# Kernel optimization log

Measured on AMD Instinct MI355X. Metric: run time of the kernel, lower is better.

The kernel has to match this reference:

```python
import jax, jax.numpy as jnp
import numpy as np

TEMPERATURE_F = 0.5  # temperature_f from __init__


def setup_inputs() -> dict:
    key = jax.random.key(0)
    k1, k2 = jax.random.split(key)
    B, D = 4096, 512
    h_i = jax.random.normal(k1, (B, D), dtype=jnp.float32)
    h_j = jax.random.normal(k2, (B, D), dtype=jnp.float32)
    return {"h_i": h_i, "h_j": h_j}


def reference(h_i, h_j) -> jnp.ndarray:
    # NT-Xent loss (forward_private). N = 2*batch_size.
    B = h_i.shape[0]
    N = 2 * B
    h = jnp.concatenate([h_i, h_j], axis=0)          # [N, D]
    sim = (h @ h.T) / TEMPERATURE_F                   # [N, N]

    # Positive pairs: sim[i, i+B] and sim[i+B, i]
    sim_i_j = jnp.diagonal(sim, offset=B)             # [B]
    sim_j_i = jnp.diagonal(sim, offset=-B)            # [B]
    pos = jnp.concatenate([sim_i_j, sim_j_i], axis=0)  # [N]

    # Original builds logits = [pos | negatives] where negatives are the row of
    # sim with the diagonal and the positive entry removed, and labels are 0.
    # Cross-entropy per row = -pos_i + logsumexp(pos_i, negatives_i)
    #                       = -pos_i + logsumexp over row i of sim excluding the
    #                         diagonal (the positive entry equals pos_i, so the
    #                         set of logsumexp'd values is identical).
    neg_inf = jnp.finfo(sim.dtype).min
    diag = jnp.eye(N, dtype=bool)
    sim_masked = jnp.where(diag, neg_inf, sim)        # exclude self-similarity
    lse = jax.nn.logsumexp(sim_masked, axis=1)        # [N]

    loss = jnp.sum(lse - pos) / N                     # CE sum reduction, / N
    return loss
```

## Files before the change

### kernel.cpp

```cpp
#include <hip/hip_runtime.h>
#include <hip/hip_bf16.h>
#include <float.h>

#define BN_ 4096
#define DD  512
#define NN  8192
#define SCALE 2.0f
#define BUF 16384

typedef unsigned short u16;
typedef __attribute__((ext_vector_type(8))) short short8;
typedef __attribute__((ext_vector_type(4))) float floatx4;

struct alignas(8) U16x4 { u16 x, y, z, w; };

__device__ __forceinline__ u16 f2bf(float f) {
    union { float f; unsigned u; } c; c.f = f;
    unsigned u = c.u;
    unsigned r = (u + 0x7fffu + ((u >> 16) & 1u)) >> 16;
    return (u16)r;
}

__device__ __forceinline__ void async_copy16(const u16* g, u16* l) {
    __builtin_amdgcn_global_load_lds(
        (const __attribute__((address_space(1))) void*)g,
        (__attribute__((address_space(3))) void*)l, 16, 0, 0);
}

__global__ __launch_bounds__(256) void convert_pos_kernel(const float* __restrict__ hi,
                                                          const float* __restrict__ hj,
                                                          u16* __restrict__ H,
                                                          float* __restrict__ Pos,
                                                          float* __restrict__ out) {
    __shared__ float red[4];
    int t = blockIdx.x * 256 + threadIdx.x;
    int e = t * 4;
    const int BD = BN_ * DD;
    float4 a = *(const float4*)(hi + e);
    float4 b = *(const float4*)(hj + e);
    U16x4 oa, ob;
    oa.x = f2bf(a.x); oa.y = f2bf(a.y); oa.z = f2bf(a.z); oa.w = f2bf(a.w);
    ob.x = f2bf(b.x); ob.y = f2bf(b.y); ob.z = f2bf(b.z); ob.w = f2bf(b.w);
    *(U16x4*)(H + e) = oa;
    *(U16x4*)(H + BD + e) = ob;
    float dot = a.x * b.x + a.y * b.y + a.z * b.z + a.w * b.w;
#pragma unroll
    for (int msk = 1; msk < 64; msk <<= 1) dot += __shfl_xor(dot, msk);
    int lane = threadIdx.x & 63, wid = threadIdx.x >> 6;
    if (lane == 0) red[wid] = dot;
    __syncthreads();
    if (threadIdx.x == 0) {
        Pos[blockIdx.x] = red[0] + red[1] + red[2] + red[3];
        if (blockIdx.x == 0) *out = 0.0f;
    }
}

#define MFMA_(va, vb, c) __builtin_amdgcn_mfma_f32_16x16x32_bf16(va, vb, c, 0, 0, 0)

#define MF_ROW(mi, areg)                       \
    acc[mi][0] = MFMA_(areg, b0, acc[mi][0]);  \
    acc[mi][1] = MFMA_(areg, b1, acc[mi][1]);  \
    acc[mi][2] = MFMA_(areg, b2, acc[mi][2]);  \
    acc[mi][3] = MFMA_(areg, b3, acc[mi][3]);

#define VMWAIT(n) asm volatile("s_waitcnt vmcnt(" #n ")" ::: "memory")

#define STAGE(gb, k0, rbase, lb) {                                              \
    async_copy16((gb) + (size_t)(rbase) * DD + (k0) + so0, (lb) + (rbase) * 64 + do0); \
    async_copy16((gb) + (size_t)(rbase) * DD + (k0) + so1, (lb) + (rbase) * 64 + do1); }

#define PHASE(cA, cB, kkq, mh, RB, STG, VMn)                     \
    {                                                            \
        short8 a0 = *(const short8*)&cA[offA[kkq][(mh)*4 + 0]];  \
        short8 a1 = *(const short8*)&cA[offA[kkq][(mh)*4 + 1]];  \
        short8 a2 = *(const short8*)&cA[offA[kkq][(mh)*4 + 2]];  \
        short8 a3 = *(const short8*)&cA[offA[kkq][(mh)*4 + 3]];  \
        if (RB) {                                                \
            b0 = *(const short8*)&cB[offB[kkq][0]];              \
            b1 = *(const short8*)&cB[offB[kkq][1]];              \
            b2 = *(const short8*)&cB[offB[kkq][2]];              \
            b3 = *(const short8*)&cB[offB[kkq][3]];              \
        }                                                        \
        STG;                                                     \
        VMWAIT(VMn);                                             \
        __builtin_amdgcn_s_barrier();                            \
        asm volatile("" ::: "memory");                           \
        __builtin_amdgcn_s_setprio(1);                           \
        MF_ROW((mh)*4 + 0, a0)                                   \
        MF_ROW((mh)*4 + 1, a1)                                   \
        MF_ROW((mh)*4 + 2, a2)                                   \
        MF_ROW((mh)*4 + 3, a3)                                   \
        __builtin_amdgcn_s_setprio(0);                           \
        __builtin_amdgcn_s_barrier();                            \
        asm volatile("" ::: "memory");                           \
    }

__global__ __launch_bounds__(512, 2) void gram_kernel(const u16* __restrict__ H,
                                                      float* __restrict__ Mpart,
                                                      float* __restrict__ Spart) {
    __shared__ u16 As[2 * BUF];
    __shared__ u16 Bs[2 * BUF];

    const int tid  = threadIdx.x;
    const int lane = tid & 63;
    const int wid  = tid >> 6;
    const int quad = lane >> 4;
    const int ln15 = lane & 15;
    const int wr = wid >> 2;
    const int wc = wid & 3;

    int t = blockIdx.x;
    int bi = (int)((sqrtf(8.0f * (float)t + 1.0f) - 1.0f) * 0.5f);
    while ((bi + 1) * (bi + 2) / 2 <= t) bi++;
    while (bi * (bi + 1) / 2 > t) bi--;
    const int bj = t - bi * (bi + 1) / 2;
    const bool diag = (bi == bj);
    const int biBase = bi * 256, bjBase = bj * 256;

    const u16* __restrict__ HA = H + (size_t)biBase * DD;
    const u16* __restrict__ HB = H + (size_t)bjBase * DD;

    const int c0 = tid, c1 = tid + 512;
    const size_t so0 = (size_t)(c0 >> 3) * DD + ((c0 & 7) ^ ((c0 >> 3) & 7)) * 8;
    const size_t so1 = (size_t)(c1 >> 3) * DD + ((c1 & 7) ^ ((c1 >> 3) & 7)) * 8;
    const int do0 = c0 * 8, do1 = c1 * 8;

    int offA[2][8], offB[2][4];
#pragma unroll
    for (int kk = 0; kk < 2; kk++) {
#pragma unroll
        for (int m = 0; m < 8; m++) {
            int r = wr * 128 + m * 16 + ln15;
            offA[kk][m] = (r * 8 + ((kk * 4 + quad) ^ (r & 7))) * 8;
        }
#pragma unroll
        for (int n = 0; n < 4; n++) {
            int r = wc * 64 + n * 16 + ln15;
            offB[kk][n] = (r * 8 + ((kk * 4 + quad) ^ (r & 7))) * 8;
        }
    }

    floatx4 acc[8][4];
#pragma unroll
    for (int i = 0; i < 8; i++)
#pragma unroll
        for (int j = 0; j < 4; j++) acc[i][j] = (floatx4)0.0f;

    STAGE(HB, 0,  0,   &Bs[0]);
    STAGE(HB, 0,  128, &Bs[0]);
    STAGE(HA, 0,  0,   &As[0]);
    STAGE(HA, 0,  128, &As[0]);
    STAGE(HB, 64, 0,   &Bs[BUF]);
    VMWAIT(4);
    __builtin_amdgcn_s_barrier();
    asm volatile("" ::: "memory");

#pragma unroll 2
    for (int kt = 0; kt < 8; ++kt) {
        u16* cA = &As[(kt & 1) * BUF];
        u16* cB = &Bs[(kt & 1) * BUF];
        u16* nA = &As[((kt + 1) & 1) * BUF];
        u16* nB = &Bs[((kt + 1) & 1) * BUF];
        int k1 = (kt + 1) * 64; if (k1 > 448) k1 = 448;
        int k2 = (kt + 2) * 64; if (k2 > 448) k2 = 448;
        short8 b0, b1, b2, b3;
        PHASE(cA, cB, 0, 0, 1, STAGE(HB, k1, 128, nB), 4)
        PHASE(cA, cB, 0, 1, 0, STAGE(HA, k1, 0,   nA), 8)
        PHASE(cA, cB, 1, 0, 1, STAGE(HA, k1, 128, nA), 8)
        PHASE(cA, cB, 1, 1, 0, STAGE(HB, k2, 0,   cB), 4)
    }

    asm volatile("s_waitcnt vmcnt(0)" ::: "memory");
    __syncthreads();

#pragma unroll
    for (int m = 0; m < 8; m++)
#pragma unroll
        for (int n = 0; n < 4; n++)
#pragma unroll
            for (int g = 0; g < 4; g++) {
                float v = SCALE * acc[m][n][g];
                if (diag) {
                    int lrow = wr * 128 + m * 16 + quad * 4 + g;
                    int lcol = wc * 64 + n * 16 + ln15;
                    if (lrow == lcol) v = -FLT_MAX;
                }
                acc[m][n][g] = v;
            }

    float* Rm = (float*)&As[0];
    float* Rs = Rm + 1024;
    float* Cm = Rs + 1024;
    float* Cs = Cm + 512;

#pragma unroll
    for (int m = 0; m < 8; m++) {
#pragma unroll
        for (int g = 0; g < 4; g++) {
            float vmax = fmaxf(fmaxf(acc[m][0][g], acc[m][1][g]),
                               fmaxf(acc[m][2][g], acc[m][3][g]));
#pragma unroll
            for (int msk = 1; msk < 16; msk <<= 1)
                vmax = fmaxf(vmax, __shfl_xor(vmax, msk));
            float s = __expf(acc[m][0][g] - vmax) + __expf(acc[m][1][g] - vmax)
                    + __expf(acc[m][2][g] - vmax) + __expf(acc[m][3][g] - vmax);
#pragma unroll
            for (int msk = 1; msk < 16; msk <<= 1) s += __shfl_xor(s, msk);
            if (ln15 == 0) {
                int x = wr * 128 + m * 16 + quad * 4 + g;
                Rm[wc * 256 + x] = vmax; Rs[wc * 256 + x] = s;
            }
        }
    }

    if (!diag) {
#pragma unroll
        for (int n = 0; n < 4; n++) {
            float cm = -FLT_MAX;
#pragma unroll
            for (int m = 0; m < 8; m++)
#pragma unroll
                for (int g = 0; g < 4; g++) cm = fmaxf(cm, acc[m][n][g]);
            cm = fmaxf(cm, __shfl_xor(cm, 16));
            cm = fmaxf(cm, __shfl_xor(cm, 32));
            float s = 0.0f;
#pragma unroll
            for (int m = 0; m < 8; m++)
#pragma unroll
                for (int g = 0; g < 4; g++) s += __expf(acc[m][n][g] - cm);
            s += __shfl_xor(s, 16);
            s += __shfl_xor(s, 32);
            if (quad == 0) {
                int y = wc * 64 + n * 16 + ln15;
                Cm[wr * 256 + y] = cm; Cs[wr * 256 + y] = s;
            }
        }
    }
    __syncthreads();

    if (tid < 256) {
        float m0 = Rm[tid], m1 = Rm[256 + tid], m2 = Rm[512 + tid], m3 = Rm[768 + tid];
        float mm = fmaxf(fmaxf(m0, m1), fmaxf(m2, m3));
        float s = Rs[tid] * __expf(m0 - mm) + Rs[256 + tid] * __expf(m1 - mm)
                + Rs[512 + tid] * __expf(m2 - mm) + Rs[768 + tid] * __expf(m3 - mm);
        Mpart[(size_t)bj * NN + biBase + tid] = mm;
        Spart[(size_t)bj * NN + biBase + tid] = s;
    } else if (!diag) {
        int y = tid - 256;
        float m0 = Cm[y], m1 = Cm[256 + y];
        float mm = fmaxf(m0, m1);
        float s = Cs[y] * __expf(m0 - mm) + Cs[256 + y] * __expf(m1 - mm);
        Mpart[(size_t)bi * NN + bjBase + y] = mm;
        Spart[(size_t)bi * NN + bjBase + y] = s;
    }
}

__global__ __launch_bounds__(256) void lse_kernel(const float* __restrict__ Mpart,
                                                  const float* __restrict__ Spart,
                                                  const float* __restrict__ Pos,
                                                  float* __restrict__ out) {
    __shared__ float sm[4][64], ss[4][64];
    __shared__ float red[256];
    int tid = threadIdx.x;
    int wid = tid >> 6, lane = tid & 63;
    int r = blockIdx.x * 64 + lane;
    float m = -FLT_MAX, s = 0.0f;
#pragma unroll
    for (int i = 0; i < 8; i++) {
        int c = wid * 8 + i;
        float mc = Mpart[(size_t)c * NN + r];
        float sc = Spart[(size_t)c * NN + r];
        float mn = fmaxf(m, mc);
        s = s * __expf(m - mn) + sc * __expf(mc - mn);
        m = mn;
    }
    sm[wid][lane] = m; ss[wid][lane] = s;
    __syncthreads();
    float v = 0.0f;
    if (tid < 64) {
        float m0 = sm[0][tid], m1 = sm[1][tid], m2 = sm[2][tid], m3 = sm[3][tid];
        float mm = fmaxf(fmaxf(m0, m1), fmaxf(m2, m3));
        float sa = ss[0][tid] * __expf(m0 - mm) + ss[1][tid] * __expf(m1 - mm)
                 + ss[2][tid] * __expf(m2 - mm) + ss[3][tid] * __expf(m3 - mm);
        v = mm + logf(sa);
        if (tid < 16) v += -4.0f * Pos[blockIdx.x * 16 + tid];
    }
    red[tid] = v;
    __syncthreads();
    for (int st = 128; st > 0; st >>= 1) {
        if (tid < st) red[tid] += red[tid + st];
        __syncthreads();
    }
    if (tid == 0) atomicAdd(out, red[0] * (1.0f / (float)NN));
}

extern "C" void kernel_launch(void* const* d_in, const int* in_sizes, int n_in,
                              void* d_out, int out_size, void* d_ws, size_t ws_size,
                              hipStream_t stream) {
    const float* hi = (const float*)d_in[0];
    const float* hj = (const float*)d_in[1];
    float* out = (float*)d_out;

    u16*   H     = (u16*)d_ws;
    float* Mpart = (float*)((char*)d_ws + (size_t)8 * 1024 * 1024);
    float* Spart = (float*)((char*)d_ws + (size_t)10 * 1024 * 1024);
    float* Pos   = (float*)((char*)d_ws + (size_t)12 * 1024 * 1024);

    convert_pos_kernel<<<2048, 256, 0, stream>>>(hi, hj, H, Pos, out);

    gram_kernel<<<528, 512, 0, stream>>>(H, Mpart, Spart);

    lse_kernel<<<128, 256, 0, stream>>>(Mpart, Spart, Pos, out);
}
```

Measured before the change: 156.9 us.

## Fuse LSE reduction into gram kernel via ticket, persistent grid, simpler pipeline

The separate lse_kernel is removed. The last 32 gram blocks to finish, identified by an atomic ticket counter, spin-wait until all blocks are done and then do the per-row logsumexp merge and the final reduction. The gram kernel now runs a persistent 512-block grid with a blockIdx swizzle that loops over the 528 triangular tiles. The four-phase interleaved K pipeline is replaced by a simpler double-buffered loop that stages whole K-slices with one barrier pair per step. This saves a kernel launch and may improve L2 locality. The costs are a second-pass tail for 16 tiles, a spin-wait that depends on every block being co-resident, and less fine-grained overlap of loads with MFMA work.

```diff
diff --git a/kernel.cpp b/kernel.cpp
--- a/kernel.cpp
+++ b/kernel.cpp
@@ -7,6 +7,9 @@
 #define NN  8192
 #define SCALE 2.0f
 #define BUF 16384
+#define NTILE 528
+#define GRIDG 512
+#define NDUTY 32
 
 typedef unsigned short u16;
 typedef __attribute__((ext_vector_type(8))) short short8;
@@ -31,7 +34,8 @@
                                                           const float* __restrict__ hj,
                                                           u16* __restrict__ H,
                                                           float* __restrict__ Pos,
-                                                          float* __restrict__ out) {
+                                                          float* __restrict__ out,
+                                                          unsigned* __restrict__ ticket) {
     __shared__ float red[4];
     int t = blockIdx.x * 256 + threadIdx.x;
     int e = t * 4;
@@ -51,7 +55,7 @@
     __syncthreads();
     if (threadIdx.x == 0) {
         Pos[blockIdx.x] = red[0] + red[1] + red[2] + red[3];
-        if (blockIdx.x == 0) *out = 0.0f;
+        if (blockIdx.x == 0) { *out = 0.0f; *ticket = 0u; }
     }
 }
 
@@ -65,41 +69,51 @@
 
 #define VMWAIT(n) asm volatile("s_waitcnt vmcnt(" #n ")" ::: "memory")
 
-#define STAGE(gb, k0, rbase, lb) {                                              \
-    async_copy16((gb) + (size_t)(rbase) * DD + (k0) + so0, (lb) + (rbase) * 64 + do0); \
-    async_copy16((gb) + (size_t)(rbase) * DD + (k0) + so1, (lb) + (rbase) * 64 + do1); }
-
-#define PHASE(cA, cB, kkq, mh, RB, STG, VMn)                     \
+#define STAGE_T(kb, pA, pB) {                          \
+    async_copy16(HA + so0 + (kb), (pA) + dd0);         \
+    async_copy16(HB + so0 + (kb), (pB) + dd0);         \
+    async_copy16(HA + so1 + (kb), (pA) + dd1);         \
+    async_copy16(HB + so1 + (kb), (pB) + dd1);         \
+    async_copy16(HA + so2 + (kb), (pA) + dd2);         \
+    async_copy16(HB + so2 + (kb), (pB) + dd2);         \
+    async_copy16(HA + so3 + (kb), (pA) + dd3);         \
+    async_copy16(HB + so3 + (kb), (pB) + dd3);         \
+}
+
+#define CKK(cA, cB, kk) {                                        \
+    short8 b0 = *(const short8*)&(cB)[offB[kk][0]];              \
+    short8 b1 = *(const short8*)&(cB)[offB[kk][1]];              \
+    short8 b2 = *(const short8*)&(cB)[offB[kk][2]];              \
+    short8 b3 = *(const short8*)&(cB)[offB[kk][3]];              \
     {                                                            \
-        short8 a0 = *(const short8*)&cA[offA[kkq][(mh)*4 + 0]];  \
-        short8 a1 = *(const short8*)&cA[offA[kkq][(mh)*4 + 1]];  \
-        short8 a2 = *(const short8*)&cA[offA[kkq][(mh)*4 + 2]];  \
-        short8 a3 = *(const short8*)&cA[offA[kkq][(mh)*4 + 3]];  \
-        if (RB) {                                                \
-            b0 = *(const short8*)&cB[offB[kkq][0]];              \
-            b1 = *(const short8*)&cB[offB[kkq][1]];              \
-            b2 = *(const short8*)&cB[offB[kkq][2]];              \
-            b3 = *(const short8*)&cB[offB[kkq][3]];              \
-        }                                                        \
-        STG;                                                     \
-        VMWAIT(VMn);                                             \
-        __builtin_amdgcn_s_barrier();                            \
-        asm volatile("" ::: "memory");                           \
-        __builtin_amdgcn_s_setprio(1);                           \
-        MF_ROW((mh)*4 + 0, a0)                                   \
-        MF_ROW((mh)*4 + 1, a1)                                   \
-        MF_ROW((mh)*4 + 2, a2)                                   \
-        MF_ROW((mh)*4 + 3, a3)                                   \
-        __builtin_amdgcn_s_setprio(0);                           \
-        __builtin_amdgcn_s_barrier();                            \
-        asm volatile("" ::: "memory");                           \
-    }
+        short8 a0 = *(const short8*)&(cA)[offA[kk][0]];          \
+        short8 a1 = *(const short8*)&(cA)[offA[kk][1]];          \
+        short8 a2 = *(const short8*)&(cA)[offA[kk][2]];          \
+        short8 a3 = *(const short8*)&(cA)[offA[kk][3]];          \
+        MF_ROW(0, a0) MF_ROW(1, a1) MF_ROW(2, a2) MF_ROW(3, a3)  \
+    }                                                            \
+    {                                                            \
+        short8 a0 = *(const short8*)&(cA)[offA[kk][4]];          \
+        short8 a1 = *(const short8*)&(cA)[offA[kk][5]];          \
+        short8 a2 = *(const short8*)&(cA)[offA[kk][6]];          \
+        short8 a3 = *(const short8*)&(cA)[offA[kk][7]];          \
+        MF_ROW(4, a0) MF_ROW(5, a1) MF_ROW(6, a2) MF_ROW(7, a3)  \
+    }                                                            \
+}
+
+#define COMPUTE(cA, cB) { CKK(cA, cB, 0) CKK(cA, cB, 1) }
+
+#define BARRIER() { __builtin_amdgcn_s_barrier(); asm volatile("" ::: "memory"); }
 
 __global__ __launch_bounds__(512, 2) void gram_kernel(const u16* __restrict__ H,
                                                       float* __restrict__ Mpart,
-                                                      float* __restrict__ Spart) {
+                                                      float* __restrict__ Spart,
+                                                      const float* __restrict__ Pos,
+                                                      float* __restrict__ out,
+                                                      unsigned* __restrict__ ticket) {
     __shared__ u16 As[2 * BUF];
     __shared__ u16 Bs[2 * BUF];
+    __shared__ unsigned shTicket;
 
     const int tid  = threadIdx.x;
     const int lane = tid & 63;
@@ -109,21 +123,14 @@
     const int wr = wid >> 2;
     const int wc = wid & 3;
 
-    int t = blockIdx.x;
-    int bi = (int)((sqrtf(8.0f * (float)t + 1.0f) - 1.0f) * 0.5f);
-    while ((bi + 1) * (bi + 2) / 2 <= t) bi++;
-    while (bi * (bi + 1) / 2 > t) bi--;
-    const int bj = t - bi * (bi + 1) / 2;
-    const bool diag = (bi == bj);
-    const int biBase = bi * 256, bjBase = bj * 256;
-
-    const u16* __restrict__ HA = H + (size_t)biBase * DD;
-    const u16* __restrict__ HB = H + (size_t)bjBase * DD;
-
-    const int c0 = tid, c1 = tid + 512;
+    const int bswz = (blockIdx.x & 7) * (GRIDG / 8) + (blockIdx.x >> 3);
+
+    const int c0 = tid, c1 = tid + 512, c2 = tid + 1024, c3 = tid + 1536;
     const size_t so0 = (size_t)(c0 >> 3) * DD + ((c0 & 7) ^ ((c0 >> 3) & 7)) * 8;
     const size_t so1 = (size_t)(c1 >> 3) * DD + ((c1 & 7) ^ ((c1 >> 3) & 7)) * 8;
-    const int do0 = c0 * 8, do1 = c1 * 8;
+    const size_t so2 = (size_t)(c2 >> 3) * DD + ((c2 & 7) ^ ((c2 >> 3) & 7)) * 8;
+    const size_t so3 = (size_t)(c3 >> 3) * DD + ((c3 & 7) ^ ((c3 >> 3) & 7)) * 8;
+    const int dd0 = c0 * 8, dd1 = c1 * 8, dd2 = c2 * 8, dd3 = c3 * 8;
 
     int offA[2][8], offB[2][4];
 #pragma unroll
@@ -140,158 +147,163 @@
         }
     }
 
-    floatx4 acc[8][4];
-#pragma unroll
-    for (int i = 0; i < 8; i++)
-#pragma unroll
-        for (int j = 0; j < 4; j++) acc[i][j] = (floatx4)0.0f;
-
-    STAGE(HB, 0,  0,   &Bs[0]);
-    STAGE(HB, 0,  128, &Bs[0]);
-    STAGE(HA, 0,  0,   &As[0]);
-    STAGE(HA, 0,  128, &As[0]);
-    STAGE(HB, 64, 0,   &Bs[BUF]);
-    VMWAIT(4);
-    __builtin_amdgcn_s_barrier();
-    asm volatile("" ::: "memory");
-
-#pragma unroll 2
-    for (int kt = 0; kt < 8; ++kt) {
-        u16* cA = &As[(kt & 1) * BUF];
-        u16* cB = &Bs[(kt & 1) * BUF];
-        u16* nA = &As[((kt + 1) & 1) * BUF];
-        u16* nB = &Bs[((kt + 1) & 1) * BUF];
-        int k1 = (kt + 1) * 64; if (k1 > 448) k1 = 448;
-        int k2 = (kt + 2) * 64; if (k2 > 448) k2 = 448;
-        short8 b0, b1, b2, b3;
-        PHASE(cA, cB, 0, 0, 1, STAGE(HB, k1, 128, nB), 4)
-        PHASE(cA, cB, 0, 1, 0, STAGE(HA, k1, 0,   nA), 8)
-        PHASE(cA, cB, 1, 0, 1, STAGE(HA, k1, 128, nA), 8)
-        PHASE(cA, cB, 1, 1, 0, STAGE(HB, k2, 0,   cB), 4)
+    for (int tile = bswz; tile < NTILE; tile += GRIDG) {
+        __syncthreads();
+
+        int t = tile;
+        int bi = (int)((sqrtf(8.0f * (float)t + 1.0f) - 1.0f) * 0.5f);
+        while ((bi + 1) * (bi + 2) / 2 <= t) bi++;
+        while (bi * (bi + 1) / 2 > t) bi--;
+        const int bj = t - bi * (bi + 1) / 2;
+        const bool diag = (bi == bj);
+        const int biBase = bi * 256, bjBase = bj * 256;
+
+        const u16* __restrict__ HA = H + (size_t)biBase * DD;
+        const u16* __restrict__ HB = H + (size_t)bjBase * DD;
+
+        floatx4 acc[8][4];
+#pragma unroll
+        for (int i = 0; i < 8; i++)
+#pragma unroll
+            for (int j = 0; j < 4; j++) acc[i][j] = (floatx4)0.0f;
+
+        STAGE_T(0,  &As[0],   &Bs[0]);
+        STAGE_T(64, &As[BUF], &Bs[BUF]);
+
+        for (int kt = 0; kt < 7; ++kt) {
+            const u16* cA = &As[(kt & 1) * BUF];
+            const u16* cB = &Bs[(kt & 1) * BUF];
+            u16* sA = &As[(kt & 1) * BUF];
+            u16* sB = &Bs[(kt & 1) * BUF];
+            VMWAIT(8);
+            BARRIER();
+            COMPUTE(cA, cB);
+            BARRIER();
+            if (kt < 6) { int kb = (kt + 2) * 64; STAGE_T(kb, sA, sB); }
+        }
+        VMWAIT(0);
+        BARRIER();
+        COMPUTE((&As[BUF]), (&Bs[BUF]));
+        __syncthreads();
+
+#pragma unroll
+        for (int m = 0; m < 8; m++)
+#pragma unroll
+            for (int n = 0; n < 4; n++)
+#pragma unroll
+                for (int g = 0; g < 4; g++) {
+                    float v = SCALE * acc[m][n][g];
+                    if (diag) {
+                        int lrow = wr * 128 + m * 16 + quad * 4 + g;
+                        int lcol = wc * 64 + n * 16 + ln15;
+                        if (lrow == lcol) v = -FLT_MAX;
+                    }
+                    acc[m][n][g] = v;
+                }
+
+        float* Rm = (float*)&As[0];
+        float* Rs = Rm + 1024;
+        float* Cm = Rs + 1024;
+        float* Cs = Cm + 512;
+
+#pragma unroll
+        for (int m = 0; m < 8; m++) {
+#pragma unroll
+            for (int g = 0; g < 4; g++) {
+                float vmax = fmaxf(fmaxf(acc[m][0][g], acc[m][1][g]),
+                                   fmaxf(acc[m][2][g], acc[m][3][g]));
+#pragma unroll
+                for (int msk = 1; msk < 16; msk <<= 1)
+                    vmax = fmaxf(vmax, __shfl_xor(vmax, msk));
+                float s = __expf(acc[m][0][g] - vmax) + __expf(acc[m][1][g] - vmax)
+                        + __expf(acc[m][2][g] - vmax) + __expf(acc[m][3][g] - vmax);
+#pragma unroll
+                for (int msk = 1; msk < 16; msk <<= 1) s += __shfl_xor(s, msk);
+                if (ln15 == 0) {
+                    int x = wr * 128 + m * 16 + quad * 4 + g;
+                    Rm[wc * 256 + x] = vmax; Rs[wc * 256 + x] = s;
+                }
+            }
+        }
+
+        if (!diag) {
+#pragma unroll
+            for (int n = 0; n < 4; n++) {
+                float cm = -FLT_MAX;
+#pragma unroll
+                for (int m = 0; m < 8; m++)
+#pragma unroll
+                    for (int g = 0; g < 4; g++) cm = fmaxf(cm, acc[m][n][g]);
+                cm = fmaxf(cm, __shfl_xor(cm, 16));
+                cm = fmaxf(cm, __shfl_xor(cm, 32));
+                float s = 0.0f;
+#pragma unroll
+                for (int m = 0; m < 8; m++)
+#pragma unroll
+                    for (int g = 0; g < 4; g++) s += __expf(acc[m][n][g] - cm);
+                s += __shfl_xor(s, 16);
+                s += __shfl_xor(s, 32);
+                if (quad == 0) {
+                    int y = wc * 64 + n * 16 + ln15;
+                    Cm[wr * 256 + y] = cm; Cs[wr * 256 + y] = s;
+                }
+            }
+        }
+        __syncthreads();
+
+        if (tid < 256) {
+            float m0 = Rm[tid], m1 = Rm[256 + tid], m2 = Rm[512 + tid], m3 = Rm[768 + tid];
+            float mm = fmaxf(fmaxf(m0, m1), fmaxf(m2, m3));
+            float s = Rs[tid] * __expf(m0 - mm) + Rs[256 + tid] * __expf(m1 - mm)
+                    + Rs[512 + tid] * __expf(m2 - mm) + Rs[768 + tid] * __expf(m3 - mm);
+            Mpart[(size_t)bj * NN + biBase + tid] = mm;
+            Spart[(size_t)bj * NN + biBase + tid] = s;
+        } else if (!diag) {
+            int y = tid - 256;
+            float m0 = Cm[y], m1 = Cm[256 + y];
+            float mm = fmaxf(m0, m1);
+            float s = Cs[y] * __expf(m0 - mm) + Cs[256 + y] * __expf(m1 - mm);
+            Mpart[(size_t)bi * NN + bjBase + y] = mm;
+            Spart[(size_t)bi * NN + bjBase + y] = s;
+        }
     }
 
-    asm volatile("s_waitcnt vmcnt(0)" ::: "memory");
+    __threadfence();
     __syncthreads();
-
-#pragma unroll
-    for (int m = 0; m < 8; m++)
-#pragma unroll
-        for (int n = 0; n < 4; n++)
-#pragma unroll
-            for (int g = 0; g < 4; g++) {
-                float v = SCALE * acc[m][n][g];
-                if (diag) {
-                    int lrow = wr * 128 + m * 16 + quad * 4 + g;
-                    int lcol = wc * 64 + n * 16 + ln15;
-                    if (lrow == lcol) v = -FLT_MAX;
-                }
-                acc[m][n][g] = v;
+    if (tid == 0) shTicket = atomicAdd(ticket, 1u);
+    __syncthreads();
+    if (shTicket >= (unsigned)(GRIDG - NDUTY)) {
+        if (tid == 0) {
+            while (atomicAdd(ticket, 0u) < (unsigned)GRIDG)
+                __builtin_amdgcn_s_sleep(2);
+        }
+        __syncthreads();
+        __threadfence();
+        const int idx = (int)shTicket - (GRIDG - NDUTY);
+        float v = 0.0f;
+        if (tid < 256) {
+            int r = idx * 256 + tid;
+            float m = -FLT_MAX, s = 0.0f;
+#pragma unroll 8
+            for (int c = 0; c < 32; c++) {
+                float mc = Mpart[(size_t)c * NN + r];
+                float sc = Spart[(size_t)c * NN + r];
+                float mn = fmaxf(m, mc);
+                s = s * __expf(m - mn) + sc * __expf(mc - mn);
+                m = mn;
             }
-
-    float* Rm = (float*)&As[0];
-    float* Rs = Rm + 1024;
-    float* Cm = Rs + 1024;
-    float* Cs = Cm + 512;
-
-#pragma unroll
-    for (int m = 0; m < 8; m++) {
-#pragma unroll
-        for (int g = 0; g < 4; g++) {
-            float vmax = fmaxf(fmaxf(acc[m][0][g], acc[m][1][g]),
-                               fmaxf(acc[m][2][g], acc[m][3][g]));
-#pragma unroll
-            for (int msk = 1; msk < 16; msk <<= 1)
-                vmax = fmaxf(vmax, __shfl_xor(vmax, msk));
-            float s = __expf(acc[m][0][g] - vmax) + __expf(acc[m][1][g] - vmax)
-                    + __expf(acc[m][2][g] - vmax) + __expf(acc[m][3][g] - vmax);
-#pragma unroll
-            for (int msk = 1; msk < 16; msk <<= 1) s += __shfl_xor(s, msk);
-            if (ln15 == 0) {
-                int x = wr * 128 + m * 16 + quad * 4 + g;
-                Rm[wc * 256 + x] = vmax; Rs[wc * 256 + x] = s;
-            }
-        }
+            v = m + logf(s);
+            if (tid < 64) v += -4.0f * Pos[idx * 64 + tid];
+        }
+        float* red = (float*)&As[0];
+        red[tid] = v;
+        __syncthreads();
+        for (int st = 256; st > 0; st >>= 1) {
+            if (tid < st) red[tid] += red[tid + st];
+            __syncthreads();
+        }
+        if (tid == 0) atomicAdd(out, red[0] * (1.0f / (float)NN));
     }
-
-    if (!diag) {
-#pragma unroll
-        for (int n = 0; n < 4; n++) {
-            float cm = -FLT_MAX;
-#pragma unroll
-            for (int m = 0; m < 8; m++)
-#pragma unroll
-                for (int g = 0; g < 4; g++) cm = fmaxf(cm, acc[m][n][g]);
-            cm = fmaxf(cm, __shfl_xor(cm, 16));
-            cm = fmaxf(cm, __shfl_xor(cm, 32));
-            float s = 0.0f;
-#pragma unroll
-            for (int m = 0; m < 8; m++)
-#pragma unroll
-                for (int g = 0; g < 4; g++) s += __expf(acc[m][n][g] - cm);
-            s += __shfl_xor(s, 16);
-            s += __shfl_xor(s, 32);
-            if (quad == 0) {
-                int y = wc * 64 + n * 16 + ln15;
-                Cm[wr * 256 + y] = cm; Cs[wr * 256 + y] = s;
-            }
-        }
-    }
-    __syncthreads();
-
-    if (tid < 256) {
-        float m0 = Rm[tid], m1 = Rm[256 + tid], m2 = Rm[512 + tid], m3 = Rm[768 + tid];
-        float mm = fmaxf(fmaxf(m0, m1), fmaxf(m2, m3));
-        float s = Rs[tid] * __expf(m0 - mm) + Rs[256 + tid] * __expf(m1 - mm)
-                + Rs[512 + tid] * __expf(m2 - mm) + Rs[768 + tid] * __expf(m3 - mm);
-        Mpart[(size_t)bj * NN + biBase + tid] = mm;
-        Spart[(size_t)bj * NN + biBase + tid] = s;
-    } else if (!diag) {
-        int y = tid - 256;
-        float m0 = Cm[y], m1 = Cm[256 + y];
-        float mm = fmaxf(m0, m1);
-        float s = Cs[y] * __expf(m0 - mm) + Cs[256 + y] * __expf(m1 - mm);
-        Mpart[(size_t)bi * NN + bjBase + y] = mm;
-        Spart[(size_t)bi * NN + bjBase + y] = s;
-    }
-}
-
-__global__ __launch_bounds__(256) void lse_kernel(const float* __restrict__ Mpart,
-                                                  const float* __restrict__ Spart,
-                                                  const float* __restrict__ Pos,
-                                                  float* __restrict__ out) {
-    __shared__ float sm[4][64], ss[4][64];
-    __shared__ float red[256];
-    int tid = threadIdx.x;
-    int wid = tid >> 6, lane = tid & 63;
-    int r = blockIdx.x * 64 + lane;
-    float m = -FLT_MAX, s = 0.0f;
-#pragma unroll
-    for (int i = 0; i < 8; i++) {
-        int c = wid * 8 + i;
-        float mc = Mpart[(size_t)c * NN + r];
-        float sc = Spart[(size_t)c * NN + r];
-        float mn = fmaxf(m, mc);
-        s = s * __expf(m - mn) + sc * __expf(mc - mn);
-        m = mn;
-    }
-    sm[wid][lane] = m; ss[wid][lane] = s;
-    __syncthreads();
-    float v = 0.0f;
-    if (tid < 64) {
-        float m0 = sm[0][tid], m1 = sm[1][tid], m2 = sm[2][tid], m3 = sm[3][tid];
-        float mm = fmaxf(fmaxf(m0, m1), fmaxf(m2, m3));
-        float sa = ss[0][tid] * __expf(m0 - mm) + ss[1][tid] * __expf(m1 - mm)
-                 + ss[2][tid] * __expf(m2 - mm) + ss[3][tid] * __expf(m3 - mm);
-        v = mm + logf(sa);
-        if (tid < 16) v += -4.0f * Pos[blockIdx.x * 16 + tid];
-    }
-    red[tid] = v;
-    __syncthreads();
-    for (int st = 128; st > 0; st >>= 1) {
-        if (tid < st) red[tid] += red[tid + st];
-        __syncthreads();
-    }
-    if (tid == 0) atomicAdd(out, red[0] * (1.0f / (float)NN));
 }
 
 extern "C" void kernel_launch(void* const* d_in, const int* in_sizes, int n_in,
@@ -301,14 +313,13 @@
     const float* hj = (const float*)d_in[1];
     float* out = (float*)d_out;
 
-    u16*   H     = (u16*)d_ws;
-    float* Mpart = (float*)((char*)d_ws + (size_t)8 * 1024 * 1024);
-    float* Spart = (float*)((char*)d_ws + (size_t)10 * 1024 * 1024);
-    float* Pos   = (float*)((char*)d_ws + (size_t)12 * 1024 * 1024);
-
-    convert_pos_kernel<<<2048, 256, 0, stream>>>(hi, hj, H, Pos, out);
-
-    gram_kernel<<<528, 512, 0, stream>>>(H, Mpart, Spart);
-
-    lse_kernel<<<128, 256, 0, stream>>>(Mpart, Spart, Pos, out);
-}
+    u16*      H      = (u16*)d_ws;
+    float*    Mpart  = (float*)((char*)d_ws + (size_t)8 * 1024 * 1024);
+    float*    Spart  = (float*)((char*)d_ws + (size_t)10 * 1024 * 1024);
+    float*    Pos    = (float*)((char*)d_ws + (size_t)12 * 1024 * 1024);
+    unsigned* ticket = (unsigned*)((char*)d_ws + (size_t)13 * 1024 * 1024);
+
+    convert_pos_kernel<<<2048, 256, 0, stream>>>(hi, hj, H, Pos, out, ticket);
+
+    gram_kernel<<<GRIDG, 512, 0, stream>>>(H, Mpart, Spart, Pos, out, ticket);
+}
```

New measurement: 233.3 us. +48.6%, slower.
